# Kernel optimization log

Measured on AMD Instinct MI355X. Metric: run time of the kernel, lower is better.

Reference implementation:

```python
import jax, jax.numpy as jnp
import numpy as np

NNZ = 819200
NUM_SESS = 16384
ITEMS_NUM = 1000000
EMB_DIM = 64


def setup_inputs() -> dict:
    key = jax.random.key(0)
    k1, k2, k3, k4 = jax.random.split(key, 4)
    row_idx = jnp.sort(jax.random.randint(k1, (NNZ,), 0, NUM_SESS, dtype=jnp.int32))
    col_idx = jax.random.randint(k2, (NNZ,), 0, ITEMS_NUM, dtype=jnp.int32)
    data_tensor = jax.random.uniform(k3, (NNZ,), dtype=jnp.float32)
    embeddings = jax.random.normal(k4, (ITEMS_NUM, EMB_DIM), dtype=jnp.float32)
    return {
        "row_idx": row_idx,
        "col_idx": col_idx,
        "data_tensor": data_tensor,
        "num_ids": NUM_SESS,
        "embeddings": embeddings,
    }


def reference(row_idx, col_idx, data_tensor, num_ids, embeddings):
    # sparse_coo([num_ids, ITEMS_NUM]) @ embeddings
    # == per-session weighted sum of gathered item embeddings.
    gathered = embeddings[col_idx]                      # [nnz, d]
    weighted = gathered * data_tensor[:, None]          # [nnz, d]
    user_embeddings = jax.ops.segment_sum(
        weighted, row_idx, num_segments=num_ids)        # [num_ids, d]
    return user_embeddings
```

## Files before the change

### kernel.cpp

```cpp
#include <hip/hip_runtime.h>


__global__ __launch_bounds__(256) void wsum_sess_kernel(
    const int*    __restrict__ row_idx,
    const int*    __restrict__ col_idx,
    const float*  __restrict__ data,
    const float4* __restrict__ emb,
    float4*       __restrict__ out,
    int nnz, int num_sess)
{
    const int wave = threadIdx.x >> 6;
    const int lane = threadIdx.x & 63;
    const int sess = (blockIdx.x << 2) + wave;
    if (sess >= num_sess) return;

    int lo = 0, hi = nnz;
    while (lo < hi) {
        int mid = (lo + hi) >> 1;
        if (row_idx[mid] < sess) lo = mid + 1; else hi = mid;
    }
    const int start = lo;
    hi = nnz;
    while (lo < hi) {
        int mid = (lo + hi) >> 1;
        if (row_idx[mid] < sess + 1) lo = mid + 1; else hi = mid;
    }
    const int end = lo;

    const int r = lane >> 4;
    const int c = lane & 15;

    float4 acc = make_float4(0.f, 0.f, 0.f, 0.f);

    int j0 = start;
    for (; j0 + 8 <= end; j0 += 8) {
        int   ja = j0 + r;
        int   jb = j0 + 4 + r;
        int   ca = col_idx[ja];
        int   cb = col_idx[jb];
        float wa = data[ja];
        float wb = data[jb];
        float4 ea = emb[(size_t)ca * 16 + c];
        float4 eb = emb[(size_t)cb * 16 + c];
        acc.x += wa * ea.x + wb * eb.x;
        acc.y += wa * ea.y + wb * eb.y;
        acc.z += wa * ea.z + wb * eb.z;
        acc.w += wa * ea.w + wb * eb.w;
    }
    for (; j0 < end; j0 += 4) {
        int   j     = j0 + r;
        bool  valid = (j < end);
        int   col   = valid ? col_idx[j] : 0;
        float w     = valid ? data[j]    : 0.f;
        float4 e = emb[(size_t)col * 16 + c];
        acc.x += w * e.x;
        acc.y += w * e.y;
        acc.z += w * e.z;
        acc.w += w * e.w;
    }

    acc.x += __shfl_xor(acc.x, 16, 64);
    acc.y += __shfl_xor(acc.y, 16, 64);
    acc.z += __shfl_xor(acc.z, 16, 64);
    acc.w += __shfl_xor(acc.w, 16, 64);
    acc.x += __shfl_xor(acc.x, 32, 64);
    acc.y += __shfl_xor(acc.y, 32, 64);
    acc.z += __shfl_xor(acc.z, 32, 64);
    acc.w += __shfl_xor(acc.w, 32, 64);

    if (r == 0)
        out[(size_t)sess * 16 + c] = acc;
}

extern "C" void kernel_launch(void* const* d_in, const int* in_sizes, int n_in,
                              void* d_out, int out_size, void* d_ws, size_t ws_size,
                              hipStream_t stream) {
    const int*   row_idx = (const int*)  d_in[0];
    const int*   col_idx = (const int*)  d_in[1];
    const float* data    = (const float*)d_in[2];
    const float* emb     = (const float*)d_in[4];

    const int nnz      = in_sizes[0];
    const int num_sess = out_size / 64;

    const int blocks = (num_sess + 3) / 4;
    wsum_sess_kernel<<<blocks, 256, 0, stream>>>(
        row_idx, col_idx, data, (const float4*)emb, (float4*)d_out,
        nnz, num_sess);
}
```

Before: 359.4 us.

## Build CSR row pointers in a pre-pass and unroll gather loop to 16

Adds a pre-pass kernel that turns the sorted row indices into a CSR row_ptr array in workspace, so each wave reads its segment bounds directly instead of running two binary searches over the whole row_idx array. The main loop is unrolled to process 16 nonzeros per iteration with four independent embedding gathers in flight, and launch bounds request higher occupancy. This costs an extra kernel launch and a pass over row_idx, and relies on the workspace being large enough for num_sess+1 ints.

```diff
diff --git a/kernel.cpp b/kernel.cpp
--- a/kernel.cpp
+++ b/kernel.cpp
@@ -1,31 +1,40 @@
 #include <hip/hip_runtime.h>
 
 
-__global__ __launch_bounds__(256) void wsum_sess_kernel(
-    const int*    __restrict__ row_idx,
+__global__ __launch_bounds__(256) void build_rowptr_kernel(
+    const int* __restrict__ row_idx,
+    int*       __restrict__ row_ptr,
+    int nnz, int num_sess)
+{
+    int j = blockIdx.x * blockDim.x + threadIdx.x;
+    if (j >= nnz) return;
+    int r = row_idx[j];
+    if (j == 0) {
+        for (int s = 0; s <= r; ++s) row_ptr[s] = 0;
+    } else {
+        int rp = row_idx[j - 1];
+        for (int s = rp + 1; s <= r; ++s) row_ptr[s] = j;
+    }
+    if (j == nnz - 1) {
+        for (int s = r + 1; s <= num_sess; ++s) row_ptr[s] = nnz;
+    }
+}
+
+__global__ __launch_bounds__(256, 8) void wsum_sess_kernel(
+    const int*    __restrict__ row_ptr,
     const int*    __restrict__ col_idx,
     const float*  __restrict__ data,
     const float4* __restrict__ emb,
     float4*       __restrict__ out,
-    int nnz, int num_sess)
+    int num_sess)
 {
     const int wave = threadIdx.x >> 6;
     const int lane = threadIdx.x & 63;
     const int sess = (blockIdx.x << 2) + wave;
     if (sess >= num_sess) return;
 
-    int lo = 0, hi = nnz;
-    while (lo < hi) {
-        int mid = (lo + hi) >> 1;
-        if (row_idx[mid] < sess) lo = mid + 1; else hi = mid;
-    }
-    const int start = lo;
-    hi = nnz;
-    while (lo < hi) {
-        int mid = (lo + hi) >> 1;
-        if (row_idx[mid] < sess + 1) lo = mid + 1; else hi = mid;
-    }
-    const int end = lo;
+    const int start = row_ptr[sess];
+    const int end   = row_ptr[sess + 1];
 
     const int r = lane >> 4;
     const int c = lane & 15;
@@ -33,26 +42,30 @@
     float4 acc = make_float4(0.f, 0.f, 0.f, 0.f);
 
     int j0 = start;
-    for (; j0 + 8 <= end; j0 += 8) {
-        int   ja = j0 + r;
-        int   jb = j0 + 4 + r;
-        int   ca = col_idx[ja];
-        int   cb = col_idx[jb];
-        float wa = data[ja];
-        float wb = data[jb];
-        float4 ea = emb[(size_t)ca * 16 + c];
-        float4 eb = emb[(size_t)cb * 16 + c];
-        acc.x += wa * ea.x + wb * eb.x;
-        acc.y += wa * ea.y + wb * eb.y;
-        acc.z += wa * ea.z + wb * eb.z;
-        acc.w += wa * ea.w + wb * eb.w;
+    for (; j0 + 16 <= end; j0 += 16) {
+        int   c0 = col_idx[j0 + 0  + r];
+        int   c1 = col_idx[j0 + 4  + r];
+        int   c2 = col_idx[j0 + 8  + r];
+        int   c3 = col_idx[j0 + 12 + r];
+        float w0 = data[j0 + 0  + r];
+        float w1 = data[j0 + 4  + r];
+        float w2 = data[j0 + 8  + r];
+        float w3 = data[j0 + 12 + r];
+        float4 e0 = emb[((size_t)c0 << 4) + c];
+        float4 e1 = emb[((size_t)c1 << 4) + c];
+        float4 e2 = emb[((size_t)c2 << 4) + c];
+        float4 e3 = emb[((size_t)c3 << 4) + c];
+        acc.x += w0 * e0.x + w1 * e1.x + w2 * e2.x + w3 * e3.x;
+        acc.y += w0 * e0.y + w1 * e1.y + w2 * e2.y + w3 * e3.y;
+        acc.z += w0 * e0.z + w1 * e1.z + w2 * e2.z + w3 * e3.z;
+        acc.w += w0 * e0.w + w1 * e1.w + w2 * e2.w + w3 * e3.w;
     }
     for (; j0 < end; j0 += 4) {
         int   j     = j0 + r;
         bool  valid = (j < end);
         int   col   = valid ? col_idx[j] : 0;
         float w     = valid ? data[j]    : 0.f;
-        float4 e = emb[(size_t)col * 16 + c];
+        float4 e = emb[((size_t)col << 4) + c];
         acc.x += w * e.x;
         acc.y += w * e.y;
         acc.z += w * e.z;
@@ -69,7 +82,7 @@
     acc.w += __shfl_xor(acc.w, 32, 64);
 
     if (r == 0)
-        out[(size_t)sess * 16 + c] = acc;
+        out[((size_t)sess << 4) + c] = acc;
 }
 
 extern "C" void kernel_launch(void* const* d_in, const int* in_sizes, int n_in,
@@ -83,8 +96,13 @@
     const int nnz      = in_sizes[0];
     const int num_sess = out_size / 64;
 
+    int* row_ptr = (int*)d_ws;
+
+    build_rowptr_kernel<<<(nnz + 255) / 256, 256, 0, stream>>>(
+        row_idx, row_ptr, nnz, num_sess);
+
     const int blocks = (num_sess + 3) / 4;
     wsum_sess_kernel<<<blocks, 256, 0, stream>>>(
-        row_idx, col_idx, data, (const float4*)emb, (float4*)d_out,
-        nnz, num_sess);
+        row_ptr, col_idx, data, (const float4*)emb, (float4*)d_out,
+        num_sess);
 }
```

Measured after the change: 325.3 us. 1.1x faster.
